# Optimization experiments

Hardware: AMD Instinct MI355X
Metric: run time of the kernel (lower is better)

Reference implementation:

```python
import jax, jax.numpy as jnp
import numpy as np

# Hyperparameters matching init_kwargs
IN_CH = 64
OUT_CH = 128
KERNEL = (3, 3)
STRIDE = (1, 1)
PADDING = 'SAME'
K_ORDER = 3          # spline order
G_INTERVALS = 3      # grid intervals
GRID_MIN, GRID_MAX = -1.0, 1.0
N_BASIS = G_INTERVALS + K_ORDER  # basis functions per input = 6
PATCH_DIM = IN_CH * KERNEL[0] * KERNEL[1]  # 576


def _grid():
    # Extended uniform knot vector: G + 2k + 1 knots
    h = (GRID_MAX - GRID_MIN) / G_INTERVALS
    return jnp.arange(-K_ORDER, G_INTERVALS + K_ORDER + 1, dtype=jnp.float32) * h + GRID_MIN


def _b_splines(x):
    # x: [N, n_in] -> bases: [N, n_in, G + k]
    grid = _grid()  # [G + 2k + 1]
    xe = x[..., None]  # [N, n_in, 1]
    bases = ((xe >= grid[:-1]) & (xe < grid[1:])).astype(x.dtype)  # order-0, [N, n_in, G+2k]
    for p in range(1, K_ORDER + 1):
        left = (xe - grid[: -(p + 1)]) / (grid[p:-1] - grid[: -(p + 1)]) * bases[..., :-1]
        right = (grid[p + 1:] - xe) / (grid[p + 1:] - grid[1:-p]) * bases[..., 1:]
        bases = left + right
    return bases  # [N, n_in, G + k]


def setup_inputs() -> dict:
    key = jax.random.key(0)
    k0, k1, k2, k3 = jax.random.split(key, 4)
    x = jax.random.normal(k0, (8, 64, 64, IN_CH), dtype=jnp.float32)
    base_w = jax.random.normal(k1, (OUT_CH, PATCH_DIM), dtype=jnp.float32) * 0.05
    spline_w = jax.random.normal(k2, (OUT_CH, PATCH_DIM, N_BASIS), dtype=jnp.float32) * 0.05
    bias = jax.random.normal(k3, (OUT_CH,), dtype=jnp.float32) * 0.05
    return {'x': x, 'base_w': base_w, 'spline_w': spline_w, 'bias': bias}


def reference(x, base_w, spline_w, bias):
    batch = x.shape[0]
    dn = ('NHWC', 'HWIO', 'NHWC')
    patches = jax.lax.conv_general_dilated_patches(
        lhs=x, filter_shape=KERNEL, window_strides=STRIDE, padding=PADDING,
        dimension_numbers=dn)  # [B, H, W, patch_dim]
    out_spatial = patches.shape[1:-1]
    p = patches.reshape(-1, PATCH_DIM)  # [N, patch_dim]
    # EfficientKAN: residual (silu) branch + spline branch + bias
    base_out = jax.nn.silu(p) @ base_w.T                      # [N, out]
    bases = _b_splines(p)                                      # [N, patch_dim, G+k]
    spline_out = jnp.einsum('nig,oig->no', bases, spline_w)    # [N, out]
    y = base_out + spline_out + bias
    return y.reshape(batch, *out_spatial, OUT_CH)
```

## Files before the change

### kernel.cpp

```cpp
#include <hip/hip_runtime.h>

typedef __attribute__((ext_vector_type(8))) short short8;
typedef __attribute__((ext_vector_type(16))) float f32x16;

#define FT2_SHORTS (512u * 4356u * 8u)
#define PLANE16    4356

typedef __attribute__((address_space(3))) unsigned int lds_u32_t;
typedef __attribute__((address_space(1))) const unsigned int g_u32_t;

__device__ __forceinline__ unsigned short f2bf(float x) {
    union { float f; unsigned u; } v; v.f = x;
    unsigned r = v.u + 0x7FFFu + ((v.u >> 16) & 1u);
    return (unsigned short)(r >> 16);
}

__device__ __forceinline__ void feat8(float p, unsigned short* uf) {
    float e   = __expf(-p);
    float sig = 1.f / (1.f + e);
    uf[0] = f2bf(p * sig);
    float u  = p * 1.5f + 4.5f;
    float fj = floorf(u);
    int   j0 = (int)fj;
    float t  = u - fj;
    bool  inr = (u >= 0.f) && (u < 9.f);
    float t2 = t * t, t3 = t2 * t;
    const float c16 = 1.f / 6.f;
    float r0 = t3 * c16;
    float r1 = (-3.f * t3 + 3.f * t2 + 3.f * t + 1.f) * c16;
    float r2 = (3.f * t3 - 6.f * t2 + 4.f) * c16;
    float s1 = 1.f - t;
    float r3 = s1 * s1 * s1 * c16;
#pragma unroll
    for (int g = 0; g < 6; ++g) {
        int r = j0 - g;
        float v = (r == 0) ? r0 : ((r == 1) ? r1 : ((r == 2) ? r2 : ((r == 3) ? r3 : 0.f)));
        uf[1 + g] = f2bf(inr ? v : 0.f);
    }
    uf[7] = 0;
}

__global__ __launch_bounds__(256)
void prep_all(const float* __restrict__ x,
              const float* __restrict__ bw, const float* __restrict__ sw,
              unsigned short* __restrict__ ft, unsigned short* __restrict__ wt) {
    const int blk = blockIdx.x;
    const int tid = threadIdx.x;

    if (tid < 144) {
        int idx = blk * 144 + tid;
        int o = idx / 576;
        int i = idx - o * 576;
        int slab = i >> 3, e = i & 7;
        union { unsigned short u[8]; uint4 v; } pk;
        pk.u[0] = f2bf(bw[o * 576 + i]);
        const float* s = sw + (size_t)(o * 576 + i) * 6;
#pragma unroll
        for (int f = 0; f < 6; ++f) pk.u[1 + f] = f2bf(s[f]);
        pk.u[7] = 0;
        *(uint4*)(wt + ((size_t)slab * 8192 + e * 1024 + o * 8)) = pk.v;
    }

    {
        short8 pad = { 0, 0, (short)0x3CAB, (short)0x3EF5,
                       (short)0x3EF5, (short)0x3CAB, 0, 0 };
        for (int t = tid; t < 260; t += 256) {
            int yy, xx;
            if (t < 66)       { yy = 0;       xx = t; }
            else if (t < 132) { yy = 65;      xx = t - 66; }
            else if (t < 196) { yy = t - 131; xx = 0; }
            else              { yy = t - 195; xx = 65; }
            ((short8*)ft)[blk * PLANE16 + yy * 66 + xx] = pad;
        }
    }

    __shared__ float Xl[64 * 65];
    const int b = blk >> 6, y = blk & 63;
    const float* xl = x + (size_t)blk * 4096;
    for (int f4 = tid; f4 < 1024; f4 += 256) {
        float4 v = ((const float4*)xl)[f4];
        int xx = f4 >> 4, c4 = (f4 & 15) << 2;
        float* d = &Xl[xx * 65 + c4];
        d[0] = v.x; d[1] = v.y; d[2] = v.z; d[3] = v.w;
    }
    __syncthreads();
    const int xx = tid & 63;
    const int cw = tid >> 6;
#pragma unroll 4
    for (int p = 0; p < 16; ++p) {
        int c = cw + (p << 2);
        float pv = Xl[xx * 65 + c];
        union { unsigned short u[8]; uint4 v; } pk;
        feat8(pv, pk.u);
        size_t o16 = (size_t)(c * 8 + b) * PLANE16 + (y + 1) * 66 + (xx + 1);
        *(uint4*)(ft + (o16 << 3)) = pk.v;
    }
}

#define STAGE_AB(sl)                                                                  \
    {                                                                                 \
        unsigned short* bufb = Bufs + (((sl) & 1) << 14);                             \
        const unsigned short* bsrc = wt + (size_t)(slab0 + (sl)) * 8192 + bsoff;      \
        unsigned short* bdst = bufb + bsoff;                                          \
        _Pragma("unroll")                                                             \
        for (int t = 0; t < 4; ++t)                                                   \
            __builtin_amdgcn_global_load_lds((g_u32_t*)(bsrc + t * 512),              \
                                             (lds_u32_t*)(bdst + t * 512), 16, 0, 0); \
        _Pragma("unroll")                                                             \
        for (int t = 0; t < 4; ++t) {                                                 \
            int idx = wave * 4 + t;                                                   \
            int ia  = (slab0 + (sl)) * 8 + (idx >> 1);                                \
            int g2  = idx & 1;                                                        \
            int c_  = (ia * 7282) >> 16;                                              \
            int i9_ = ia - c_ * 9;                                                    \
            int kh_ = (i9_ * 11) >> 5;                                                \
            int kw_ = i9_ - kh_ * 3;                                                  \
            const unsigned short* asrc = ft +                                         \
                (((size_t)(c_ * 8 + b) * PLANE16 + (y0 + g2 + kh_) * 66 + kw_) << 3)  \
                + lane * 8;                                                           \
            unsigned short* adst = bufb + 8192 + idx * 512 + lane * 8;                \
            __builtin_amdgcn_global_load_lds((g_u32_t*)asrc, (lds_u32_t*)adst,        \
                                             16, 0, 0);                               \
        }                                                                             \
    }

#define KSTEP(s_)                                                                     \
    {                                                                                 \
        int iloc = 2 * (s_) + h;                                                      \
        const unsigned short* Ab = bufr + 8192 + (iloc * 2 + g) * 512;                \
        const unsigned short* Bb = bufr + iloc * 1024;                                \
        short8 a0 = *(const short8*)(Ab + l32 * 8);                                   \
        short8 a1 = *(const short8*)(Ab + (32 + l32) * 8);                            \
        short8 b0 = *(const short8*)(Bb + (nh * 64 + l32) * 8);                       \
        short8 b1 = *(const short8*)(Bb + (nh * 64 + 32 + l32) * 8);                  \
        acc00 = __builtin_amdgcn_mfma_f32_32x32x16_bf16(a0, b0, acc00, 0, 0, 0);      \
        acc01 = __builtin_amdgcn_mfma_f32_32x32x16_bf16(a0, b1, acc01, 0, 0, 0);      \
        acc10 = __builtin_amdgcn_mfma_f32_32x32x16_bf16(a1, b0, acc10, 0, 0, 0);      \
        acc11 = __builtin_amdgcn_mfma_f32_32x32x16_bf16(a1, b1, acc11, 0, 0, 0);      \
    }

__global__ __launch_bounds__(256, 2)
void convkan_gemm(const unsigned short* __restrict__ ft,
                  const unsigned short* __restrict__ wt,
                  const float* __restrict__ bias,
                  float* __restrict__ out) {
    extern __shared__ unsigned short Bufs[];

    const int tid  = threadIdx.x;
    const int blk  = blockIdx.x;
    const int kk   = blk & 1;
    const int mb   = blk >> 1;
    const int lane = tid & 63;
    const int wave = tid >> 6;
    const int g    = wave >> 1;
    const int nh   = wave & 1;
    const int l32  = lane & 31;
    const int h    = lane >> 5;

    const int b  = mb >> 5;
    const int y0 = (mb & 31) << 1;
    const int slab0 = kk * 36;

    const int bsoff = wave * 2048 + lane * 8;

    f32x16 acc00, acc01, acc10, acc11;
#pragma unroll
    for (int e = 0; e < 16; ++e) { acc00[e] = 0.f; acc01[e] = 0.f; acc10[e] = 0.f; acc11[e] = 0.f; }

    STAGE_AB(0);
    __syncthreads();

    for (int it = 0; it < 36; ++it) {
        if (it + 1 < 36) STAGE_AB(it + 1);
        const unsigned short* bufr = Bufs + ((it & 1) << 14);
        KSTEP(0) KSTEP(1) KSTEP(2) KSTEP(3)
        __syncthreads();
    }

    const float bv0 = kk ? 0.f : bias[nh * 64 + l32];
    const float bv1 = kk ? 0.f : bias[nh * 64 + 32 + l32];
    const int prow = (mb * 2 + g) * 64;
    const int ncol = nh * 64 + l32;
#pragma unroll
    for (int r = 0; r < 16; ++r) {
        int mrow = (r & 3) + ((r >> 2) << 3) + 4 * h;
        float* p0 = out + (size_t)(prow + mrow) * 128 + ncol;
        float* p1 = out + (size_t)(prow + 32 + mrow) * 128 + ncol;
        atomicAdd(p0,      acc00[r] + bv0);
        atomicAdd(p0 + 32, acc01[r] + bv1);
        atomicAdd(p1,      acc10[r] + bv0);
        atomicAdd(p1 + 32, acc11[r] + bv1);
    }
}

extern "C" void kernel_launch(void* const* d_in, const int* in_sizes, int n_in,
                              void* d_out, int out_size, void* d_ws, size_t ws_size,
                              hipStream_t stream) {
    (void)in_sizes; (void)n_in; (void)ws_size;
    const float* x        = (const float*)d_in[0];
    const float* base_w   = (const float*)d_in[1];
    const float* spline_w = (const float*)d_in[2];
    const float* bias     = (const float*)d_in[3];
    float* out = (float*)d_out;

    unsigned short* ft = (unsigned short*)d_ws;
    unsigned short* wt = ft + FT2_SHORTS;

    hipMemsetAsync(out, 0, (size_t)out_size * sizeof(float), stream);
    hipLaunchKernelGGL(prep_all, dim3(512), dim3(256), 0, stream,
                       x, base_w, spline_w, ft, wt);

    const int shmem = 2 * 16384 * 2;
    (void)hipFuncSetAttribute((const void*)convkan_gemm,
                              hipFuncAttributeMaxDynamicSharedMemorySize, shmem);
    hipLaunchKernelGGL(convkan_gemm, dim3(512), dim3(256), shmem, stream,
                       ft, wt, bias, out);
}
```

Measured before the change: 149.2 us.

## Enlarge GEMM tile to four output rows with triple-buffered LDS pipeline

Each block now covers four image rows using 512 threads and 8 waves, so every staged weight slab is shared by twice as many output rows. The double buffer with __syncthreads is replaced by three LDS stages, explicit vmcnt waits and raw barriers, plus s_setprio around the MFMA section, which lets loads run further ahead of compute. The cost is more LDS per block (144 KB), half as many blocks (256), and reliance on hand-counted vmcnt values being correct.

```diff
diff --git a/kernel.cpp b/kernel.cpp
--- a/kernel.cpp
+++ b/kernel.cpp
@@ -97,20 +97,23 @@
     }
 }
 
-#define STAGE_AB(sl)                                                                  \
+#define BUF_SHORTS 24576
+
+#define STAGE(sl, q_)                                                                 \
     {                                                                                 \
-        unsigned short* bufb = Bufs + (((sl) & 1) << 14);                             \
-        const unsigned short* bsrc = wt + (size_t)(slab0 + (sl)) * 8192 + bsoff;      \
-        unsigned short* bdst = bufb + bsoff;                                          \
+        unsigned short* bufq = Bufs + (q_) * BUF_SHORTS;                              \
+        const unsigned short* bsrc = wt + (size_t)(slab0 + (sl)) * 8192;              \
         _Pragma("unroll")                                                             \
-        for (int t = 0; t < 4; ++t)                                                   \
-            __builtin_amdgcn_global_load_lds((g_u32_t*)(bsrc + t * 512),              \
-                                             (lds_u32_t*)(bdst + t * 512), 16, 0, 0); \
+        for (int r = 0; r < 2; ++r) {                                                 \
+            int boff = (r * 8 + wave) * 512 + lane * 8;                               \
+            __builtin_amdgcn_global_load_lds((g_u32_t*)(bsrc + boff),                 \
+                                             (lds_u32_t*)(bufq + boff), 16, 0, 0);    \
+        }                                                                             \
         _Pragma("unroll")                                                             \
         for (int t = 0; t < 4; ++t) {                                                 \
-            int idx = wave * 4 + t;                                                   \
-            int ia  = (slab0 + (sl)) * 8 + (idx >> 1);                                \
-            int g2  = idx & 1;                                                        \
+            int idx = wave * 4 + t;                         \
+            int ia  = (slab0 + (sl)) * 8 + (idx >> 2);                                \
+            int g2  = idx & 3;                                                        \
             int c_  = (ia * 7282) >> 16;                                              \
             int i9_ = ia - c_ * 9;                                                    \
             int kh_ = (i9_ * 11) >> 5;                                                \
@@ -118,7 +121,7 @@
             const unsigned short* asrc = ft +                                         \
                 (((size_t)(c_ * 8 + b) * PLANE16 + (y0 + g2 + kh_) * 66 + kw_) << 3)  \
                 + lane * 8;                                                           \
-            unsigned short* adst = bufb + 8192 + idx * 512 + lane * 8;                \
+            unsigned short* adst = bufq + 8192 + idx * 512 + lane * 8;                \
             __builtin_amdgcn_global_load_lds((g_u32_t*)asrc, (lds_u32_t*)adst,        \
                                              16, 0, 0);                               \
         }                                                                             \
@@ -127,7 +130,7 @@
 #define KSTEP(s_)                                                                     \
     {                                                                                 \
         int iloc = 2 * (s_) + h;                                                      \
-        const unsigned short* Ab = bufr + 8192 + (iloc * 2 + g) * 512;                \
+        const unsigned short* Ab = bufr + 8192 + (iloc * 4 + g) * 512;                \
         const unsigned short* Bb = bufr + iloc * 1024;                                \
         short8 a0 = *(const short8*)(Ab + l32 * 8);                                   \
         short8 a1 = *(const short8*)(Ab + (32 + l32) * 8);                            \
@@ -139,7 +142,22 @@
         acc11 = __builtin_amdgcn_mfma_f32_32x32x16_bf16(a1, b1, acc11, 0, 0, 0);      \
     }
 
-__global__ __launch_bounds__(256, 2)
+#define PHASE(it_, q_, n_, dostage_)                                                  \
+    {                                                                                 \
+        asm volatile("s_waitcnt vmcnt(" #n_ ")" ::: "memory");                        \
+        __builtin_amdgcn_s_barrier();                                                 \
+        asm volatile("" ::: "memory");                                                \
+        const unsigned short* bufr = Bufs + (q_) * BUF_SHORTS;                        \
+        __builtin_amdgcn_s_setprio(1);                                                \
+        KSTEP(0) KSTEP(1) KSTEP(2) KSTEP(3)                                           \
+        __builtin_amdgcn_s_setprio(0);                                                \
+        asm volatile("" ::: "memory");                                                \
+        __builtin_amdgcn_s_barrier();                                                 \
+        asm volatile("" ::: "memory");                                                \
+        if (dostage_) STAGE((it_) + 3, q_);                                           \
+    }
+
+__global__ __launch_bounds__(512, 2)
 void convkan_gemm(const unsigned short* __restrict__ ft,
                   const unsigned short* __restrict__ wt,
                   const float* __restrict__ bias,
@@ -157,29 +175,31 @@
     const int l32  = lane & 31;
     const int h    = lane >> 5;
 
-    const int b  = mb >> 5;
-    const int y0 = (mb & 31) << 1;
+    const int b  = mb >> 4;
+    const int y0 = (mb & 15) << 2;
     const int slab0 = kk * 36;
 
-    const int bsoff = wave * 2048 + lane * 8;
-
     f32x16 acc00, acc01, acc10, acc11;
 #pragma unroll
     for (int e = 0; e < 16; ++e) { acc00[e] = 0.f; acc01[e] = 0.f; acc10[e] = 0.f; acc11[e] = 0.f; }
 
-    STAGE_AB(0);
-    __syncthreads();
-
-    for (int it = 0; it < 36; ++it) {
-        if (it + 1 < 36) STAGE_AB(it + 1);
-        const unsigned short* bufr = Bufs + ((it & 1) << 14);
-        KSTEP(0) KSTEP(1) KSTEP(2) KSTEP(3)
-        __syncthreads();
-    }
+    STAGE(0, 0);
+    STAGE(1, 1);
+    STAGE(2, 2);
+
+    for (int it3 = 0; it3 < 11; ++it3) {
+        const int it = it3 * 3;
+        PHASE(it + 0, 0, 12, true)
+        PHASE(it + 1, 1, 12, true)
+        PHASE(it + 2, 2, 12, true)
+    }
+    PHASE(33, 0, 12, false)
+    PHASE(34, 1, 6,  false)
+    PHASE(35, 2, 0,  false)
 
     const float bv0 = kk ? 0.f : bias[nh * 64 + l32];
     const float bv1 = kk ? 0.f : bias[nh * 64 + 32 + l32];
-    const int prow = (mb * 2 + g) * 64;
+    const int prow = (mb * 4 + g) * 64;
     const int ncol = nh * 64 + l32;
 #pragma unroll
     for (int r = 0; r < 16; ++r) {
@@ -210,9 +230,9 @@
     hipLaunchKernelGGL(prep_all, dim3(512), dim3(256), 0, stream,
                        x, base_w, spline_w, ft, wt);
 
-    const int shmem = 2 * 16384 * 2;
+    const int shmem = 3 * BUF_SHORTS * 2;
     (void)hipFuncSetAttribute((const void*)convkan_gemm,
                               hipFuncAttributeMaxDynamicSharedMemorySize, shmem);
-    hipLaunchKernelGGL(convkan_gemm, dim3(512), dim3(256), shmem, stream,
+    hipLaunchKernelGGL(convkan_gemm, dim3(256), dim3(512), shmem, stream,
                        ft, wt, bias, out);
 }
```

Result: no change. 146.8 us (-1.6%).
